# Kernel optimization log

Measured on AMD Instinct MI355X. Metric: run time of the kernel, lower is better.

## Reference

```python
import jax, jax.numpy as jnp
import numpy as np

# Static per-expert capacities (tokens are laid out contiguously per expert)
CAPS = [1024, 512, 1024, 256, 1024, 512, 128, 1024, 512, 1024, 256, 512, 1024, 128, 64, 512]
TOTAL = sum(CAPS)  # 9536
E, H, I = 16, 1024, 4096
OFFSETS = np.concatenate([[0], np.cumsum(CAPS)])


def setup_inputs() -> dict:
    key = jax.random.key(0)
    ks = jax.random.split(key, 5)
    x = jax.random.normal(ks[0], (TOTAL, H), dtype=jnp.float32)
    W1 = jax.random.normal(ks[1], (E, I, H), dtype=jnp.float32) * 0.02
    b1 = jax.random.normal(ks[2], (E, I), dtype=jnp.float32) * 0.02
    W2 = jax.random.normal(ks[3], (E, H, I), dtype=jnp.float32) * 0.02
    b2 = jax.random.normal(ks[4], (E, H), dtype=jnp.float32) * 0.02
    return {"x": x, "W1": W1, "b1": b1, "W2": W2, "b2": b2}


def reference(x, W1, b1, W2, b2):
    # Grouped GEMM FFN: expert e processes rows [OFFSETS[e]:OFFSETS[e+1]]
    # out = gelu(x_e @ W1[e].T + b1[e]) @ W2[e].T + b2[e]
    outs = []
    for e in range(E):  # fixed, static loop over experts (capacities are static)
        xs = x[OFFSETS[e]:OFFSETS[e + 1]]                      # [cap_e, H]
        h = jax.nn.gelu(xs @ W1[e].T + b1[e], approximate=False)  # [cap_e, I]
        outs.append(h @ W2[e].T + b2[e])                       # [cap_e, H]
    return jnp.concatenate(outs, axis=0)                       # [TOTAL, H]
```

## Files before the change

kernel.cpp:

```cpp
#include <hip/hip_runtime.h>
#include <math.h>

typedef __attribute__((ext_vector_type(8))) short short8;
typedef __attribute__((ext_vector_type(4))) float f32x4;
typedef __attribute__((ext_vector_type(2))) unsigned int u32x2;
typedef __attribute__((ext_vector_type(4))) unsigned int u32x4;

#define E_NUM 16
constexpr int CAPS[E_NUM] = {1024,512,1024,256,1024,512,128,1024,512,1024,256,512,1024,128,64,512};
constexpr int OFFS[E_NUM] = {0,1024,1536,2560,2816,3840,4352,4480,5504,6016,7040,7296,7808,8832,8960,9024};
constexpr int cdiv_(int a, int b){ return (a + b - 1) / b; }
constexpr int ilog2_(int v){ int l = 0; while ((1 << l) < v) ++l; return l; }

__device__ __forceinline__ unsigned int cvt_pk_bf16(float a, float b){
  unsigned int r;
  asm("v_cvt_pk_bf16_f32 %0, %1, %2" : "=v"(r) : "v"(a), "v"(b));
  return r;
}

typedef __attribute__((address_space(1))) const unsigned char gas_u8;
typedef __attribute__((address_space(3))) unsigned char las_u8;
__device__ __forceinline__ void gl_lds16(const void* g, void* l){
  __builtin_amdgcn_global_load_lds((gas_u8*)g, (las_u8*)l, 16, 0, 0);
}

__global__ __launch_bounds__(256) void cvt_bf16_kernel(const float* __restrict__ x,
                                                       unsigned short* __restrict__ xb, int n8)
{
  int i = blockIdx.x * blockDim.x + threadIdx.x;
  const int stride = gridDim.x * blockDim.x;
  for (; i < n8; i += stride) {
    f32x4 a = *reinterpret_cast<const f32x4*>(x + (size_t)i * 8);
    f32x4 b = *reinterpret_cast<const f32x4*>(x + (size_t)i * 8 + 4);
    u32x2 lo, hi;
    lo[0] = cvt_pk_bf16(a[0], a[1]); lo[1] = cvt_pk_bf16(a[2], a[3]);
    hi[0] = cvt_pk_bf16(b[0], b[1]); hi[1] = cvt_pk_bf16(b[2], b[3]);
    *reinterpret_cast<u32x2*>(xb + (size_t)i * 8)     = lo;
    *reinterpret_cast<u32x2*>(xb + (size_t)i * 8 + 4) = hi;
  }
}

template<int NDIM, int KDIM, int LOG_GN, int NWG>
__global__ __launch_bounds__(512, 2)
void g1_gemm256(const unsigned short* __restrict__ Ah, const float* __restrict__ W,
                const float* __restrict__ bias, unsigned short* __restrict__ Oh)
{
  constexpr int A_BYTES = 256 * 64;
  constexpr int B_BYTES = 256 * 128;
  constexpr int BUF  = A_BYTES + B_BYTES;
  constexpr int GN   = 1 << LOG_GN;
  constexpr int NTT  = KDIM / 32;
  static_assert(NWG % 8 == 0);
  static_assert(NTT >= 3);

  __shared__ __align__(16) char smem[3 * BUF];

  const int tid  = threadIdx.x;
  const int braw = blockIdx.x;
  const int tt = (braw & 7) * (NWG / 8) + (braw >> 3);

  int m0 = 0, n0 = 0, Me = 0, tok0 = 0;
  size_t wbase = 0, bbase = 0;
  {
    int acc0 = 0;
    #pragma unroll
    for (int i = 0; i < E_NUM; ++i) {
      const int mt  = cdiv_(CAPS[i], 256);
      const int lmt = ilog2_(mt);
      const int nb  = mt * (NDIM / 256);
      if (tt >= acc0 && tt < acc0 + nb) {
        const int loc = tt - acc0;
        const int g   = loc >> (lmt + LOG_GN);
        const int rem = loc & ((mt << LOG_GN) - 1);
        m0   = (rem >> LOG_GN) * 256;
        n0   = ((g << LOG_GN) | (rem & (GN - 1))) * 256;
        Me   = CAPS[i];
        tok0 = OFFS[i];
        wbase = (size_t)i * NDIM * KDIM;
        bbase = (size_t)i * NDIM;
      }
      acc0 += nb;
    }
  }
  const float* Wb = W + wbase;

  const int lane = tid & 63;
  const int wv   = tid >> 6;

  auto stageA = [&](int buf, int kt) {
    const unsigned short* Ag = Ah + (size_t)(tok0 + m0) * KDIM + kt * 32;
    char* dst0 = smem + buf * BUF;
    #pragma unroll
    for (int j = 0; j < 2; ++j) {
      const int rbase = j * 128 + wv * 16;
      const int r     = rbase + (lane >> 2);
      const int blk   = (lane & 3) ^ (r & 3);
      gl_lds16((const void*)(Ag + (size_t)r * KDIM + blk * 8), (void*)(dst0 + rbase * 64));
    }
  };
  auto stageB = [&](int buf, int kt) {
    const float* Bg = Wb + (size_t)n0 * KDIM + kt * 32;
    char* dst0 = smem + buf * BUF + A_BYTES;
    #pragma unroll
    for (int j = 0; j < 4; ++j) {
      const int rbase = j * 64 + wv * 8;
      const int r     = rbase + (lane >> 3);
      const int blk   = (lane & 7) ^ (r & 7);
      gl_lds16((const void*)(Bg + (size_t)r * KDIM + blk * 4), (void*)(dst0 + rbase * 128));
    }
  };

  const int wm   = (wv >> 2) * 128;
  const int wn   = (wv & 3) * 64;
  const int lrow = lane & 15;
  const int pa0  = (((lane >> 4) ^ (lane & 3)) << 4);
  const int pb0  = ((((lane >> 4) << 1) ^ (lane & 7)) << 4);

  f32x4 acc_[8][4];
  #pragma unroll
  for (int i = 0; i < 8; ++i)
    #pragma unroll
    for (int j = 0; j < 4; ++j)
      acc_[i][j] = (f32x4){0.f, 0.f, 0.f, 0.f};

  auto compute = [&](int cur) {
    const char* ab  = smem + cur * BUF;
    const char* bbp = smem + cur * BUF + A_BYTES;
    short8 bfr[4];
    #pragma unroll
    for (int f = 0; f < 4; ++f) {
      const char* rowp = bbp + (size_t)(wn + f * 16 + lrow) * 128;
      f32x4 lo = *reinterpret_cast<const f32x4*>(rowp + pb0);
      f32x4 hi = *reinterpret_cast<const f32x4*>(rowp + (pb0 ^ 16));
      u32x4 pk;
      pk[0] = cvt_pk_bf16(lo[0], lo[1]); pk[1] = cvt_pk_bf16(lo[2], lo[3]);
      pk[2] = cvt_pk_bf16(hi[0], hi[1]); pk[3] = cvt_pk_bf16(hi[2], hi[3]);
      bfr[f] = __builtin_bit_cast(short8, pk);
    }
    #pragma unroll
    for (int i = 0; i < 8; ++i) {
      short8 afr = *reinterpret_cast<const short8*>(ab + (wm + i * 16 + lrow) * 64 + pa0);
      #pragma unroll
      for (int j = 0; j < 4; ++j)
        acc_[i][j] = __builtin_amdgcn_mfma_f32_16x16x32_bf16(afr, bfr[j], acc_[i][j], 0, 0, 0);
    }
  };

  stageA(0, 0); stageB(0, 0);
  stageA(1, 1); stageB(1, 1);
  int cur = 0, nx2 = 2;
  for (int kt = 0; kt < NTT; ++kt) {
    if (kt + 1 < NTT) asm volatile("s_waitcnt vmcnt(6)\n\ts_barrier" ::: "memory");
    else              asm volatile("s_waitcnt vmcnt(0)\n\ts_barrier" ::: "memory");
    __builtin_amdgcn_sched_barrier(0);
    if (kt + 2 < NTT) { stageA(nx2, kt + 2); stageB(nx2, kt + 2); }
    compute(cur);
    cur = (cur == 2) ? 0 : cur + 1;
    nx2 = (nx2 == 2) ? 0 : nx2 + 1;
  }

  float bv[4];
  #pragma unroll
  for (int f = 0; f < 4; ++f)
    bv[f] = bias[bbase + n0 + wn + f * 16 + lrow];

  __syncthreads();
  unsigned short* hout = (unsigned short*)smem;
  #pragma unroll
  for (int i = 0; i < 8; ++i) {
    const int rbase = wm + i * 16 + (lane >> 4) * 4;
    #pragma unroll
    for (int j = 0; j < 4; ++j) {
      #pragma unroll
      for (int jj = 0; jj < 4; ++jj) {
        float xv = acc_[i][j][jj] + bv[j];
        float y2 = xv * (1.5957691216057308f + 0.07135481627f * xv * xv);
        float g  = xv * __builtin_amdgcn_rcpf(1.0f + __expf(-y2));
        hout[(rbase + jj) * 256 + wn + j * 16 + lrow] = (unsigned short)(cvt_pk_bf16(g, g) & 0xFFFFu);
      }
    }
  }
  __syncthreads();
  #pragma unroll
  for (int s = 0; s < 16; ++s) {
    const int row = s * 16 + (tid >> 5);
    const int c   = (tid & 31) * 8;
    if (m0 + row < Me) {
      *reinterpret_cast<short8*>(Oh + (size_t)(tok0 + m0 + row) * NDIM + n0 + c)
        = *reinterpret_cast<const short8*>(hout + row * 256 + c);
    }
  }
}

template<int NDIM, int KDIM, int NWG, int KS>
__global__ __launch_bounds__(256, 5)
void g2_gemm128b(const unsigned short* __restrict__ Ah, const unsigned short* __restrict__ Wh,
                 const float* __restrict__ bias, float* __restrict__ Of)
{
  constexpr int T_BYTES = 128 * 64;
  constexpr int BUF  = 2 * T_BYTES;
  constexpr int NT   = KDIM / (KS * 32);
  constexpr int NWG1 = NWG / KS;
  static_assert(NWG % 8 == 0);
  static_assert(NT >= 2);

  __shared__ __align__(16) char smem[2 * BUF];

  const int tid  = threadIdx.x;
  const int braw = blockIdx.x;
  const int t = (braw & 7) * (NWG / 8) + (braw >> 3);

  const int kc    = t / NWG1;
  const int tt    = t % NWG1;
  const int kbase = kc * (KDIM / KS);

  int m0 = 0, n0 = 0, Me = 0, tok0 = 0;
  size_t wbase = 0, bbase = 0;
  {
    int acc0 = 0;
    #pragma unroll
    for (int i = 0; i < E_NUM; ++i) {
      const int mt = cdiv_(CAPS[i], 128);
      const int nb = mt * (NDIM / 128);
      if (tt >= acc0 && tt < acc0 + nb) {
        const int loc = tt - acc0;
        m0   = (loc & (mt - 1)) * 128;
        n0   = (loc >> ilog2_(mt)) * 128;
        Me   = CAPS[i];
        tok0 = OFFS[i];
        wbase = (size_t)i * NDIM * KDIM;
        bbase = (size_t)i * NDIM;
      }
      acc0 += nb;
    }
  }

  const int lane = tid & 63;
  const int wv   = tid >> 6;
  const int wm   = (wv >> 1) * 64;
  const int wn   = (wv & 1) * 64;
  const int lrow = lane & 15;
  const int pa0  = (((lane >> 4) ^ (lane & 3)) << 4);

  const unsigned short* Abase = Ah + (size_t)(tok0 + m0) * KDIM + kbase;
  const unsigned short* Bbase = Wh + wbase + (size_t)n0 * KDIM + kbase;

  auto stage_tile = [&](const unsigned short* base, char* dst0, int kt) {
    const unsigned short* Tg = base + kt * 32;
    #pragma unroll
    for (int j = 0; j < 2; ++j) {
      const int rbase = wv * 32 + j * 16;
      const int r     = rbase + (lane >> 2);
      const int blk   = (lane & 3) ^ (r & 3);
      gl_lds16((const void*)(Tg + (size_t)r * KDIM + blk * 8), (void*)(dst0 + rbase * 64));
    }
  };
  auto stage = [&](int buf, int kt) {
    stage_tile(Abase, smem + buf * BUF, kt);
    stage_tile(Bbase, smem + buf * BUF + T_BYTES, kt);
  };

  f32x4 acc_[4][4];
  #pragma unroll
  for (int i = 0; i < 4; ++i)
    #pragma unroll
    for (int j = 0; j < 4; ++j)
      acc_[i][j] = (f32x4){0.f, 0.f, 0.f, 0.f};

  auto compute = [&](int cur) {
    const char* ab = smem + cur * BUF;
    const char* bb = smem + cur * BUF + T_BYTES;
    short8 afr[4], bfr[4];
    #pragma unroll
    for (int f = 0; f < 4; ++f)
      afr[f] = *reinterpret_cast<const short8*>(ab + (wm + f * 16 + lrow) * 64 + pa0);
    #pragma unroll
    for (int f = 0; f < 4; ++f)
      bfr[f] = *reinterpret_cast<const short8*>(bb + (wn + f * 16 + lrow) * 64 + pa0);
    #pragma unroll
    for (int i = 0; i < 4; ++i)
      #pragma unroll
      for (int j = 0; j < 4; ++j)
        acc_[i][j] = __builtin_amdgcn_mfma_f32_16x16x32_bf16(afr[i], bfr[j], acc_[i][j], 0, 0, 0);
  };

  stage(0, 0);
  __syncthreads();
  for (int kt = 0; kt < NT; ++kt) {
    const int cur = kt & 1;
    if (kt + 1 < NT) stage(cur ^ 1, kt + 1);
    compute(cur);
    __syncthreads();
  }

  float bv[4];
  #pragma unroll
  for (int f = 0; f < 4; ++f)
    bv[f] = bias[bbase + n0 + wn + f * 16 + lrow];

  constexpr float BS = 1.0f / (float)KS;
  #pragma unroll
  for (int i = 0; i < 4; ++i) {
    const int rbase = wm + i * 16 + (lane >> 4) * 4;
    #pragma unroll
    for (int jj = 0; jj < 4; ++jj) {
      int grow = m0 + rbase + jj;
      if (grow < Me) {
        #pragma unroll
        for (int j = 0; j < 4; ++j) {
          float v = acc_[i][j][jj] + bv[j] * BS;
          float* p = Of + (size_t)(tok0 + grow) * NDIM + n0 + wn + j * 16 + lrow;
          if constexpr (KS > 1) unsafeAtomicAdd(p, v);
          else                  *p = v;
        }
      }
    }
  }
}

extern "C" void kernel_launch(void* const* d_in, const int* in_sizes, int n_in,
                              void* d_out, int out_size, void* d_ws, size_t ws_size,
                              hipStream_t stream)
{
  const float* x  = (const float*)d_in[0];
  const float* W1 = (const float*)d_in[1];
  const float* b1 = (const float*)d_in[2];
  const float* W2 = (const float*)d_in[3];
  const float* b2 = (const float*)d_in[4];
  float* out = (float*)d_out;

  constexpr size_t H_BYTES   = (size_t)9536 * 4096 * 2;
  constexpr size_t XB_BYTES  = (size_t)9536 * 1024 * 2;
  unsigned short* h   = (unsigned short*)d_ws;
  unsigned short* xb  = (unsigned short*)((char*)d_ws + H_BYTES);
  unsigned short* w2b = (unsigned short*)((char*)d_ws + H_BYTES + XB_BYTES);

  hipMemsetAsync(d_out, 0, (size_t)out_size * sizeof(float), stream);

  cvt_bf16_kernel<<<2048, 256, 0, stream>>>(x, xb, 9536 * 1024 / 8);

  g1_gemm256<4096, 1024, 2, 624><<<624, 512, 0, stream>>>(xb, W1, b1, h);

  cvt_bf16_kernel<<<2048, 256, 0, stream>>>(W2, w2b, 16 * 1024 * 4096 / 8);

  g2_gemm128b<1024, 4096, 1200, 2><<<1200, 256, 0, stream>>>(h, w2b, b2, out);
}
```

Before: 424.8 us.

## Drop split-K in second GEMM and use a three-stage LDS pipeline

The second GEMM no longer splits K across two workgroups with atomic adds. Each workgroup now runs the full K loop and writes its output directly, which also removes the output memset. The main loop becomes a triple-buffered pipeline: it keeps two tiles in flight and syncs with vmcnt-based waits and one barrier per iteration instead of two syncthreads. In exchange the grid halves to 600 workgroups (fewer waves to hide latency), and the launch bound drops to 3 blocks per SM to make room for the larger LDS footprint.

```diff
diff --git a/kernel.cpp b/kernel.cpp
--- a/kernel.cpp
+++ b/kernel.cpp
@@ -192,27 +192,22 @@
   }
 }
 
-template<int NDIM, int KDIM, int NWG, int KS>
-__global__ __launch_bounds__(256, 5)
-void g2_gemm128b(const unsigned short* __restrict__ Ah, const unsigned short* __restrict__ Wh,
+template<int NDIM, int KDIM, int NWG>
+__global__ __launch_bounds__(256, 3)
+void g2_gemm128c(const unsigned short* __restrict__ Ah, const unsigned short* __restrict__ Wh,
                  const float* __restrict__ bias, float* __restrict__ Of)
 {
   constexpr int T_BYTES = 128 * 64;
   constexpr int BUF  = 2 * T_BYTES;
-  constexpr int NT   = KDIM / (KS * 32);
-  constexpr int NWG1 = NWG / KS;
+  constexpr int NT   = KDIM / 32;
   static_assert(NWG % 8 == 0);
-  static_assert(NT >= 2);
-
-  __shared__ __align__(16) char smem[2 * BUF];
+  static_assert(NT >= 3);
+
+  __shared__ __align__(16) char smem[3 * BUF];
 
   const int tid  = threadIdx.x;
   const int braw = blockIdx.x;
-  const int t = (braw & 7) * (NWG / 8) + (braw >> 3);
-
-  const int kc    = t / NWG1;
-  const int tt    = t % NWG1;
-  const int kbase = kc * (KDIM / KS);
+  const int tt = (braw & 7) * (NWG / 8) + (braw >> 3);
 
   int m0 = 0, n0 = 0, Me = 0, tok0 = 0;
   size_t wbase = 0, bbase = 0;
@@ -242,8 +237,8 @@
   const int lrow = lane & 15;
   const int pa0  = (((lane >> 4) ^ (lane & 3)) << 4);
 
-  const unsigned short* Abase = Ah + (size_t)(tok0 + m0) * KDIM + kbase;
-  const unsigned short* Bbase = Wh + wbase + (size_t)n0 * KDIM + kbase;
+  const unsigned short* Abase = Ah + (size_t)(tok0 + m0) * KDIM;
+  const unsigned short* Bbase = Wh + wbase + (size_t)n0 * KDIM;
 
   auto stage_tile = [&](const unsigned short* base, char* dst0, int kt) {
     const unsigned short* Tg = base + kt * 32;
@@ -285,12 +280,16 @@
   };
 
   stage(0, 0);
-  __syncthreads();
+  stage(1, 1);
+  int cur = 0, nx2 = 2;
   for (int kt = 0; kt < NT; ++kt) {
-    const int cur = kt & 1;
-    if (kt + 1 < NT) stage(cur ^ 1, kt + 1);
+    if (kt + 1 < NT) asm volatile("s_waitcnt vmcnt(4)\n\ts_barrier" ::: "memory");
+    else             asm volatile("s_waitcnt vmcnt(0)\n\ts_barrier" ::: "memory");
+    __builtin_amdgcn_sched_barrier(0);
+    if (kt + 2 < NT) stage(nx2, kt + 2);
     compute(cur);
-    __syncthreads();
+    cur = (cur == 2) ? 0 : cur + 1;
+    nx2 = (nx2 == 2) ? 0 : nx2 + 1;
   }
 
   float bv[4];
@@ -298,7 +297,6 @@
   for (int f = 0; f < 4; ++f)
     bv[f] = bias[bbase + n0 + wn + f * 16 + lrow];
 
-  constexpr float BS = 1.0f / (float)KS;
   #pragma unroll
   for (int i = 0; i < 4; ++i) {
     const int rbase = wm + i * 16 + (lane >> 4) * 4;
@@ -308,10 +306,7 @@
       if (grow < Me) {
         #pragma unroll
         for (int j = 0; j < 4; ++j) {
-          float v = acc_[i][j][jj] + bv[j] * BS;
-          float* p = Of + (size_t)(tok0 + grow) * NDIM + n0 + wn + j * 16 + lrow;
-          if constexpr (KS > 1) unsafeAtomicAdd(p, v);
-          else                  *p = v;
+          Of[(size_t)(tok0 + grow) * NDIM + n0 + wn + j * 16 + lrow] = acc_[i][j][jj] + bv[j];
         }
       }
     }
@@ -335,13 +330,11 @@
   unsigned short* xb  = (unsigned short*)((char*)d_ws + H_BYTES);
   unsigned short* w2b = (unsigned short*)((char*)d_ws + H_BYTES + XB_BYTES);
 
-  hipMemsetAsync(d_out, 0, (size_t)out_size * sizeof(float), stream);
-
   cvt_bf16_kernel<<<2048, 256, 0, stream>>>(x, xb, 9536 * 1024 / 8);
 
   g1_gemm256<4096, 1024, 2, 624><<<624, 512, 0, stream>>>(xb, W1, b1, h);
 
   cvt_bf16_kernel<<<2048, 256, 0, stream>>>(W2, w2b, 16 * 1024 * 4096 / 8);
 
-  g2_gemm128b<1024, 4096, 1200, 2><<<1200, 256, 0, stream>>>(h, w2b, b2, out);
-}
+  g2_gemm128c<1024, 4096, 600><<<600, 256, 0, stream>>>(h, w2b, b2, out);
+}
```

New measurement: 358.5 us. 1.19x faster.
